# Optimization experiments

Measured on AMD Instinct MI355X. Metric: run time of the kernel, lower is better.

The kernel has to match this reference:

```python
import jax, jax.numpy as jnp
import numpy as np

N_VERT = 20000


def _gather_pad(feat, adj):
    # feat: [B, N, C]; adj: [B, N, K] with 1-based indices, 0 = padding (-> zeros)
    B, N, C = feat.shape
    padded = jnp.concatenate([jnp.zeros((B, 1, C), feat.dtype), feat], axis=1)  # [B, N+1, C]
    return jax.vmap(lambda p, a: p[a])(padded, adj)  # [B, N, K, C]


def setup_inputs() -> dict:
    key = jax.random.key(0)
    ks = jax.random.split(key, 7)
    B, N, K, M, C, O = 4, N_VERT, 16, 9, 64, 64
    x = jax.random.normal(ks[0], (B, N, C), jnp.float32)
    adj = jax.random.randint(ks[1], (B, N, K), 0, N + 1, jnp.int32)  # 0 == no neighbor
    W = jax.random.normal(ks[2], (M, O, C), jnp.float32) * 0.1
    b = jax.random.normal(ks[3], (O,), jnp.float32) * 0.1
    u = jax.random.normal(ks[4], (M, C), jnp.float32) * 0.1
    v = jax.random.normal(ks[5], (M, C), jnp.float32) * 0.1
    c = jax.random.normal(ks[6], (M,), jnp.float32) * 0.1
    return {"x": x, "adj": adj, "W": W, "b": b, "u": u, "v": v, "c": c}


def reference(x, adj, W, b, u, v, c):
    # FEAST graph conv, non-invariant path.
    mask = adj != 0  # [B, N, K]
    # attention logits: u.x_i + v.x_j + c, masked (padding) neighbors -> 0 + c
    ux = jnp.einsum('bnc,mc->bnm', x, u)          # [B, N, M]
    vx = jnp.einsum('bnc,mc->bnm', x, v)          # [B, N, M]
    vxn = _gather_pad(vx, adj)                    # [B, N, K, M]
    logits = jnp.where(mask[..., None], ux[:, :, None, :] + vxn, 0.0) + c
    q = jax.nn.softmax(logits, axis=-1)           # softmax over M kernels
    # gather raw neighbor features (zero for padding), contract q over K first,
    # then apply per-kernel W (linear, so order is equivalent to original wx-gather)
    xn = _gather_pad(x, adj)                      # [B, N, K, C]
    s = jnp.einsum('bnkm,bnkc->bnmc', q, xn)      # [B, N, M, C]
    out = jnp.einsum('bnmc,moc->bno', s, W)       # [B, N, O]
    deg = jnp.sum(mask, axis=-1).astype(x.dtype)  # [B, N]
    inv_deg = jnp.where(deg > 0, 1.0 / jnp.maximum(deg, 1.0), 0.0)
    return out * inv_deg[..., None] + b
```

## Files before the change

### kernel.cpp

```cpp
#include <hip/hip_runtime.h>
#include <cstdint>
#include <cstddef>

#define BB 4
#define NN 20000
#define KK 16
#define MM 9
#define CC 64
#define OO 64
#define BN (BB*NN)
#define MC (MM*CC)
#define UVP 12
#define QNP 160
#define QTAIL 128
#define NKS (MC/32)
#define NCHUNK16 1250

typedef _Float16 f16x8 __attribute__((ext_vector_type(8)));
typedef _Float16 f16x4 __attribute__((ext_vector_type(4)));
typedef __fp16   fp16v2 __attribute__((ext_vector_type(2)));
typedef float    f32x4 __attribute__((ext_vector_type(4)));
typedef unsigned short u16;
typedef unsigned int   u32;

union Hcv { _Float16 h; u16 u; };
__device__ __forceinline__ u16 f2h(float f) { Hcv t; t.h = (_Float16)f; return t.u; }
__device__ __forceinline__ float h2f(u16 h) { Hcv t; t.u = h; return (float)t.h; }

__global__ __launch_bounds__(256) void pre_kernel(
    const float* __restrict__ x, const float* __restrict__ W,
    const float* __restrict__ u, const float* __restrict__ v,
    const float* __restrict__ c,
    float* __restrict__ uxc, float* __restrict__ vxp,
    u16* __restrict__ xh, u16* __restrict__ wfb2)
{
    const int bid = blockIdx.x;
    if (bid >= 1250) {
        int base = (bid - 1250) * 1024 + threadIdx.x * 4;
        ushort4 wv;
        u16* wp = (u16*)&wv;
        #pragma unroll
        for (int t = 0; t < 4; ++t) {
            int i = base + t;
            int j = i & 7, o = (i >> 3) & 63, l2 = (i >> 9) & 3, ks = i >> 11;
            int kf = ks * 32 + l2 * 8 + j;
            int m = kf >> 6, cc2 = kf & 63;
            wp[t] = f2h(W[m * 4096 + o * 64 + cc2]);
        }
        *(ushort4*)(wfb2 + base) = wv;
        return;
    }
    const int wave = threadIdx.x >> 6, lane = threadIdx.x & 63;
    const int lr = lane & 15, lhi = lane >> 4;
    const int t0n = bid * 64 + wave * 16;

    const float* xr = x + (size_t)(t0n + lr) * 64 + lhi * 8;
    float xf[16];
    *(float4*)(xf + 0)  = *(const float4*)(xr + 0);
    *(float4*)(xf + 4)  = *(const float4*)(xr + 4);
    *(float4*)(xf + 8)  = *(const float4*)(xr + 32);
    *(float4*)(xf + 12) = *(const float4*)(xr + 36);
    union { u16 us[8]; f16x8 v; ushort4 s4[2]; } H0, L0, H1, L1;
    #pragma unroll
    for (int i = 0; i < 8; ++i) {
        u16 h = f2h(xf[i]);      H0.us[i] = h;  L0.us[i] = f2h(xf[i] - h2f(h));
        u16 h2 = f2h(xf[8 + i]); H1.us[i] = h2; L1.us[i] = f2h(xf[8 + i] - h2f(h2));
    }
    *(ushort4*)(xh + (size_t)(t0n + lr) * 64 + lhi * 8)      = H0.s4[0];
    *(ushort4*)(xh + (size_t)(t0n + lr) * 64 + lhi * 8 + 4)  = H0.s4[1];
    *(ushort4*)(xh + (size_t)(t0n + lr) * 64 + 32 + lhi * 8)     = H1.s4[0];
    *(ushort4*)(xh + (size_t)(t0n + lr) * 64 + 32 + lhi * 8 + 4) = H1.s4[1];

    f32x4 acc0 = {0.f,0.f,0.f,0.f}, acc1 = {0.f,0.f,0.f,0.f};
    #pragma unroll
    for (int t = 0; t < 2; ++t) {
        int r = t * 16 + lr;
        const float* gp = (r < 9) ? (u + r * 64) : (v + (r - 9) * 64);
        bool nz = r < 18;
        f32x4 acc = {0.f,0.f,0.f,0.f};
        #pragma unroll
        for (int s = 0; s < 2; ++s) {
            float gf[8];
            *(float4*)(gf + 0) = nz ? *(const float4*)(gp + s * 32 + lhi * 8)
                                    : make_float4(0.f,0.f,0.f,0.f);
            *(float4*)(gf + 4) = nz ? *(const float4*)(gp + s * 32 + lhi * 8 + 4)
                                    : make_float4(0.f,0.f,0.f,0.f);
            union { u16 us[8]; f16x8 v; } GH, GL;
            #pragma unroll
            for (int i = 0; i < 8; ++i) {
                u16 h = f2h(gf[i]); GH.us[i] = h; GL.us[i] = f2h(gf[i] - h2f(h));
            }
            f16x8 as  = s ? H1.v : H0.v;
            f16x8 asl = s ? L1.v : L0.v;
            acc = __builtin_amdgcn_mfma_f32_16x16x32_f16(as,  GH.v, acc, 0, 0, 0);
            acc = __builtin_amdgcn_mfma_f32_16x16x32_f16(as,  GL.v, acc, 0, 0, 0);
            acc = __builtin_amdgcn_mfma_f32_16x16x32_f16(asl, GH.v, acc, 0, 0, 0);
        }
        if (t == 0) acc0 = acc; else acc1 = acc;
    }
    float cv = (lr < 9) ? c[lr] : 0.f;
    #pragma unroll
    for (int reg = 0; reg < 4; ++reg) {
        int node = t0n + lhi * 4 + reg;
        if (lr < 9) uxc[(size_t)node * UVP + lr] = acc0[reg] + cv;
        else        vxp[(size_t)node * UVP + (lr - 9)] = acc0[reg];
        if (lr < 2) vxp[(size_t)node * UVP + 7 + lr] = acc1[reg];
    }
}

__global__ __launch_bounds__(256, 6) void fused_kernel(
    const u16* __restrict__ xh, const int* __restrict__ adj,
    const float* __restrict__ uxc, const float* __restrict__ vxp,
    const u16* __restrict__ wfb2, const float* __restrict__ bias,
    float* __restrict__ out)
{
    __shared__ __align__(16) u16 qlds[16 * QNP + QTAIL];
    __shared__ __align__(16) u16 slds[72 * 16 * 8];
    const int bid = blockIdx.x;
    const int grp = bid & 7;
    const int b = grp >> 1;
    const int chunk = (bid >> 3) * 2 + (grp & 1);
    const int tid = threadIdx.x, wave = tid >> 6, lane = tid & 63;
    const int lr = lane & 15, lhi = lane >> 4;
    const int node0 = b * NN + chunk * 16;
    const int rowbase = b * NN;
    const u16* xhb = xh + ((size_t)rowbase << 6);

    int jj = adj[(size_t)node0 * KK + tid];

    f16x8 aLo[4], aHi[4];
    #pragma unroll
    for (int g2 = 0; g2 < 4; ++g2) {
        int e = __builtin_amdgcn_ds_bpermute((g2 * 16 + lr) * 4, jj);
        int erow = ((e > 0) ? e : 1) - 1;
        const u16* rp = xhb + ((size_t)erow << 6) + lhi * 8;
        aLo[g2] = *(const f16x8*)(rp);
        aHi[g2] = *(const f16x8*)(rp + 32);
    }

    {
        unsigned long long bal = __ballot(jj != 0);
        int deg = __popcll((bal >> (lhi * 16)) & 0xffffull);
        float inv = (deg > 0) ? (1.0f / (float)deg) : 0.0f;
        const int node = node0 + wave * 4 + lhi;
        float q[MM];
        #pragma unroll
        for (int m = 0; m < MM; ++m) q[m] = 0.f;
        if (jj != 0) {
            const float4* ur = (const float4*)(uxc + (size_t)node * UVP);
            const float4* vr = (const float4*)(vxp + ((size_t)rowbase + (jj - 1)) * UVP);
            float4 u0 = ur[0], u1 = ur[1], u2 = ur[2];
            float4 v0 = vr[0], v1 = vr[1], v2 = vr[2];
            float l[MM] = { u0.x+v0.x, u0.y+v0.y, u0.z+v0.z, u0.w+v0.w,
                            u1.x+v1.x, u1.y+v1.y, u1.z+v1.z, u1.w+v1.w,
                            u2.x+v2.x };
            float mx = l[0];
            #pragma unroll
            for (int m = 1; m < MM; ++m) mx = fmaxf(mx, l[m]);
            float sum = 0.f;
            #pragma unroll
            for (int m = 0; m < MM; ++m) { l[m] = __expf(l[m] - mx); sum += l[m]; }
            float sc = inv / sum;
            #pragma unroll
            for (int m = 0; m < MM; ++m) q[m] = l[m] * sc;
        }
        u16* qw = qlds + (wave * 4 + lhi) * QNP + lr;
        #pragma unroll
        for (int m = 0; m < MM; ++m) qw[m * 16] = f2h(q[m]);
    }

    f16x4 qf[4];
    #pragma unroll
    for (int g2 = 0; g2 < 4; ++g2)
        qf[g2] = *(const f16x4*)(qlds + (wave * 4 + g2) * QNP + lr * 16 + lhi * 4);

    f16x8 idf[2];
    #pragma unroll
    for (int s = 0; s < 2; ++s) {
        union { u16 us[8]; f16x8 v; } t;
        #pragma unroll
        for (int j = 0; j < 8; ++j)
            t.us[j] = (lhi * 8 + j == s * 16 + lr) ? (u16)0x3C00 : (u16)0;
        idf[s] = t.v;
    }

    #pragma unroll
    for (int g2 = 0; g2 < 4; ++g2) {
        const int rnode = wave * 4 + g2;
        #pragma unroll
        for (int cc = 0; cc < 4; ++cc) {
            f32x4 xt = {0.f,0.f,0.f,0.f};
            xt = __builtin_amdgcn_mfma_f32_16x16x32_f16(
                     (cc < 2) ? aLo[g2] : aHi[g2], idf[cc & 1], xt, 0, 0, 0);
            union { fp16v2 h2[2]; f16x4 h4; } at;
            at.h2[0] = __builtin_amdgcn_cvt_pkrtz(xt[0], xt[1]);
            at.h2[1] = __builtin_amdgcn_cvt_pkrtz(xt[2], xt[3]);
            f32x4 d2 = {0.f,0.f,0.f,0.f};
            d2 = __builtin_amdgcn_mfma_f32_16x16x16f16(at.h4, qf[g2], d2, 0, 0, 0);
            if (lr < 9) {
                u32 lo = __builtin_amdgcn_perm((u32)f2h(d2[1]), (u32)f2h(d2[0]), 0x05040100u);
                u32 hi = __builtin_amdgcn_perm((u32)f2h(d2[3]), (u32)f2h(d2[2]), 0x05040100u);
                int q_ = lr * 8 + cc * 2 + (lhi >> 1);
                int idx16 = (((q_ * 16 + rnode) << 3) ^ ((lr & 7) << 3)) + (lhi & 1) * 4;
                *(uint2*)(slds + idx16) = make_uint2(lo, hi);
            }
        }
    }
    __syncthreads();

    const int o0 = wave * 16;
    float bv = bias[o0 + lr];
    f32x4 acc = {0.f,0.f,0.f,0.f};
    #pragma unroll
    for (int ks = 0; ks < NKS; ++ks) {
        int q_ = ks * 4 + lhi;
        int idx16 = ((q_ * 16 + lr) << 3) ^ (((q_ >> 3) & 7) << 3);
        f16x8 afrag = *(const f16x8*)(slds + idx16);
        f16x8 bfrag = *(const f16x8*)(wfb2 + (size_t)(((ks * 4 + lhi) * 64) + o0 + lr) * 8);
        acc = __builtin_amdgcn_mfma_f32_16x16x32_f16(afrag, bfrag, acc, 0, 0, 0);
    }
    #pragma unroll
    for (int reg = 0; reg < 4; ++reg) {
        int rr = node0 + lhi * 4 + reg;
        out[(size_t)rr * OO + o0 + lr] = acc[reg] + bv;
    }
}

extern "C" void kernel_launch(void* const* d_in, const int* in_sizes, int n_in,
                              void* d_out, int out_size, void* d_ws, size_t ws_size,
                              hipStream_t stream)
{
    const float* x   = (const float*)d_in[0];
    const int*   adj = (const int*)  d_in[1];
    const float* W   = (const float*)d_in[2];
    const float* b   = (const float*)d_in[3];
    const float* u   = (const float*)d_in[4];
    const float* v   = (const float*)d_in[5];
    const float* c   = (const float*)d_in[6];
    float* out = (float*)d_out;

    float* uxc = (float*)d_ws;
    float* vxp = uxc + (size_t)BN * UVP;
    u16*   xh  = (u16*)(vxp + (size_t)BN * UVP);
    u16*   wfb2= xh + (size_t)BN * CC;

    pre_kernel<<<1286, 256, 0, stream>>>(x, W, u, v, c, uxc, vxp, xh, wfb2);
    fused_kernel<<<5000, 256, 0, stream>>>(xh, adj, uxc, vxp, wfb2, b, out);
}
```

Measured before the change: 131.8 us.

## Fuse attention logits into main kernel and process 32 nodes per block

Moves the u·x and v·x projections out of the pre-kernel and computes the attention logits inside the fused kernel with MFMA on the already gathered fp16 neighbor rows. This removes the uxc/vxp workspace arrays and their scattered global reads. Softmax now runs across lanes with shuffles, and q is transposed through LDS with ds_read_b64_tr_b16. Each block now handles 32 nodes, so every W fragment load feeds two MFMAs and half as many blocks launch. In exchange, occupancy drops, LDS use grows, and the logits are computed in single fp16 rather than the earlier hi/lo split, which loses precision.

```diff
diff --git a/kernel.cpp b/kernel.cpp
--- a/kernel.cpp
+++ b/kernel.cpp
@@ -10,11 +10,8 @@
 #define OO 64
 #define BN (BB*NN)
 #define MC (MM*CC)
-#define UVP 12
-#define QNP 160
-#define QTAIL 128
 #define NKS (MC/32)
-#define NCHUNK16 1250
+#define NCH 625
 
 typedef _Float16 f16x8 __attribute__((ext_vector_type(8)));
 typedef _Float16 f16x4 __attribute__((ext_vector_type(4)));
@@ -25,16 +22,29 @@
 
 union Hcv { _Float16 h; u16 u; };
 __device__ __forceinline__ u16 f2h(float f) { Hcv t; t.h = (_Float16)f; return t.u; }
-__device__ __forceinline__ float h2f(u16 h) { Hcv t; t.u = h; return (float)t.h; }
 
 __global__ __launch_bounds__(256) void pre_kernel(
     const float* __restrict__ x, const float* __restrict__ W,
     const float* __restrict__ u, const float* __restrict__ v,
-    const float* __restrict__ c,
-    float* __restrict__ uxc, float* __restrict__ vxp,
-    u16* __restrict__ xh, u16* __restrict__ wfb2)
+    u16* __restrict__ xh, u16* __restrict__ wfb2, u16* __restrict__ uvfa)
 {
     const int bid = blockIdx.x;
+    if (bid == 1286) {
+        int i0 = threadIdx.x * 8;
+        u16 w8[8];
+        #pragma unroll
+        for (int tt = 0; tt < 8; ++tt) {
+            int i = i0 + tt;
+            int t = i >> 10, l = (i >> 4) & 63, s = (i >> 3) & 1, j = i & 7;
+            int m = l & 15, hh = l >> 4;
+            const float* src = t ? v : u;
+            float val = (m < 9) ? src[m * 64 + s * 32 + hh * 8 + j] : 0.f;
+            w8[tt] = f2h(val);
+        }
+        *(ushort4*)(uvfa + i0)     = *(ushort4*)(w8);
+        *(ushort4*)(uvfa + i0 + 4) = *(ushort4*)(w8 + 4);
+        return;
+    }
     if (bid >= 1250) {
         int base = (bid - 1250) * 1024 + threadIdx.x * 4;
         ushort4 wv;
@@ -53,126 +63,67 @@
     const int wave = threadIdx.x >> 6, lane = threadIdx.x & 63;
     const int lr = lane & 15, lhi = lane >> 4;
     const int t0n = bid * 64 + wave * 16;
-
     const float* xr = x + (size_t)(t0n + lr) * 64 + lhi * 8;
     float xf[16];
     *(float4*)(xf + 0)  = *(const float4*)(xr + 0);
     *(float4*)(xf + 4)  = *(const float4*)(xr + 4);
     *(float4*)(xf + 8)  = *(const float4*)(xr + 32);
     *(float4*)(xf + 12) = *(const float4*)(xr + 36);
-    union { u16 us[8]; f16x8 v; ushort4 s4[2]; } H0, L0, H1, L1;
+    union { u16 us[8]; ushort4 s4[2]; } H0, H1;
     #pragma unroll
     for (int i = 0; i < 8; ++i) {
-        u16 h = f2h(xf[i]);      H0.us[i] = h;  L0.us[i] = f2h(xf[i] - h2f(h));
-        u16 h2 = f2h(xf[8 + i]); H1.us[i] = h2; L1.us[i] = f2h(xf[8 + i] - h2f(h2));
-    }
-    *(ushort4*)(xh + (size_t)(t0n + lr) * 64 + lhi * 8)      = H0.s4[0];
-    *(ushort4*)(xh + (size_t)(t0n + lr) * 64 + lhi * 8 + 4)  = H0.s4[1];
-    *(ushort4*)(xh + (size_t)(t0n + lr) * 64 + 32 + lhi * 8)     = H1.s4[0];
-    *(ushort4*)(xh + (size_t)(t0n + lr) * 64 + 32 + lhi * 8 + 4) = H1.s4[1];
-
-    f32x4 acc0 = {0.f,0.f,0.f,0.f}, acc1 = {0.f,0.f,0.f,0.f};
-    #pragma unroll
-    for (int t = 0; t < 2; ++t) {
-        int r = t * 16 + lr;
-        const float* gp = (r < 9) ? (u + r * 64) : (v + (r - 9) * 64);
-        bool nz = r < 18;
-        f32x4 acc = {0.f,0.f,0.f,0.f};
-        #pragma unroll
-        for (int s = 0; s < 2; ++s) {
-            float gf[8];
-            *(float4*)(gf + 0) = nz ? *(const float4*)(gp + s * 32 + lhi * 8)
-                                    : make_float4(0.f,0.f,0.f,0.f);
-            *(float4*)(gf + 4) = nz ? *(const float4*)(gp + s * 32 + lhi * 8 + 4)
-                                    : make_float4(0.f,0.f,0.f,0.f);
-            union { u16 us[8]; f16x8 v; } GH, GL;
-            #pragma unroll
-            for (int i = 0; i < 8; ++i) {
-                u16 h = f2h(gf[i]); GH.us[i] = h; GL.us[i] = f2h(gf[i] - h2f(h));
-            }
-            f16x8 as  = s ? H1.v : H0.v;
-            f16x8 asl = s ? L1.v : L0.v;
-            acc = __builtin_amdgcn_mfma_f32_16x16x32_f16(as,  GH.v, acc, 0, 0, 0);
-            acc = __builtin_amdgcn_mfma_f32_16x16x32_f16(as,  GL.v, acc, 0, 0, 0);
-            acc = __builtin_amdgcn_mfma_f32_16x16x32_f16(asl, GH.v, acc, 0, 0, 0);
-        }
-        if (t == 0) acc0 = acc; else acc1 = acc;
-    }
-    float cv = (lr < 9) ? c[lr] : 0.f;
-    #pragma unroll
-    for (int reg = 0; reg < 4; ++reg) {
-        int node = t0n + lhi * 4 + reg;
-        if (lr < 9) uxc[(size_t)node * UVP + lr] = acc0[reg] + cv;
-        else        vxp[(size_t)node * UVP + (lr - 9)] = acc0[reg];
-        if (lr < 2) vxp[(size_t)node * UVP + 7 + lr] = acc1[reg];
-    }
+        H0.us[i] = f2h(xf[i]);
+        H1.us[i] = f2h(xf[8 + i]);
+    }
+    u16* xw = xh + (size_t)(t0n + lr) * 64 + lhi * 8;
+    *(ushort4*)(xw)          = H0.s4[0];
+    *(ushort4*)(xw + 4)      = H0.s4[1];
+    *(ushort4*)(xw + 32)     = H1.s4[0];
+    *(ushort4*)(xw + 32 + 4) = H1.s4[1];
 }
 
-__global__ __launch_bounds__(256, 6) void fused_kernel(
+__global__ __launch_bounds__(256, 3) void fused_kernel(
     const u16* __restrict__ xh, const int* __restrict__ adj,
-    const float* __restrict__ uxc, const float* __restrict__ vxp,
-    const u16* __restrict__ wfb2, const float* __restrict__ bias,
+    const u16* __restrict__ wfb2, const u16* __restrict__ uvfa,
+    const float* __restrict__ cvec, const float* __restrict__ bias,
     float* __restrict__ out)
 {
-    __shared__ __align__(16) u16 qlds[16 * QNP + QTAIL];
-    __shared__ __align__(16) u16 slds[72 * 16 * 8];
+    __shared__ __align__(16) u16 qlds[32 * 256];
+    __shared__ __align__(16) u16 slds[72 * 32 * 8];
     const int bid = blockIdx.x;
     const int grp = bid & 7;
     const int b = grp >> 1;
     const int chunk = (bid >> 3) * 2 + (grp & 1);
+    if (chunk >= NCH) return;
     const int tid = threadIdx.x, wave = tid >> 6, lane = tid & 63;
     const int lr = lane & 15, lhi = lane >> 4;
-    const int node0 = b * NN + chunk * 16;
-    const int rowbase = b * NN;
-    const u16* xhb = xh + ((size_t)rowbase << 6);
-
-    int jj = adj[(size_t)node0 * KK + tid];
-
-    f16x8 aLo[4], aHi[4];
-    #pragma unroll
-    for (int g2 = 0; g2 < 4; ++g2) {
-        int e = __builtin_amdgcn_ds_bpermute((g2 * 16 + lr) * 4, jj);
-        int erow = ((e > 0) ? e : 1) - 1;
-        const u16* rp = xhb + ((size_t)erow << 6) + lhi * 8;
-        aLo[g2] = *(const f16x8*)(rp);
-        aHi[g2] = *(const f16x8*)(rp + 32);
-    }
-
-    {
-        unsigned long long bal = __ballot(jj != 0);
-        int deg = __popcll((bal >> (lhi * 16)) & 0xffffull);
-        float inv = (deg > 0) ? (1.0f / (float)deg) : 0.0f;
-        const int node = node0 + wave * 4 + lhi;
-        float q[MM];
-        #pragma unroll
-        for (int m = 0; m < MM; ++m) q[m] = 0.f;
-        if (jj != 0) {
-            const float4* ur = (const float4*)(uxc + (size_t)node * UVP);
-            const float4* vr = (const float4*)(vxp + ((size_t)rowbase + (jj - 1)) * UVP);
-            float4 u0 = ur[0], u1 = ur[1], u2 = ur[2];
-            float4 v0 = vr[0], v1 = vr[1], v2 = vr[2];
-            float l[MM] = { u0.x+v0.x, u0.y+v0.y, u0.z+v0.z, u0.w+v0.w,
-                            u1.x+v1.x, u1.y+v1.y, u1.z+v1.z, u1.w+v1.w,
-                            u2.x+v2.x };
-            float mx = l[0];
-            #pragma unroll
-            for (int m = 1; m < MM; ++m) mx = fmaxf(mx, l[m]);
-            float sum = 0.f;
-            #pragma unroll
-            for (int m = 0; m < MM; ++m) { l[m] = __expf(l[m] - mx); sum += l[m]; }
-            float sc = inv / sum;
-            #pragma unroll
-            for (int m = 0; m < MM; ++m) q[m] = l[m] * sc;
-        }
-        u16* qw = qlds + (wave * 4 + lhi) * QNP + lr;
-        #pragma unroll
-        for (int m = 0; m < MM; ++m) qw[m * 16] = f2h(q[m]);
-    }
-
-    f16x4 qf[4];
-    #pragma unroll
-    for (int g2 = 0; g2 < 4; ++g2)
-        qf[g2] = *(const f16x4*)(qlds + (wave * 4 + g2) * QNP + lr * 16 + lhi * 4);
+    const int node0 = b * NN + chunk * 32;
+    const u16* xhb = xh + ((size_t)(b * NN) << 6);
+
+    int jjA[2];
+    jjA[0] = adj[(size_t)node0 * KK + tid];
+    jjA[1] = adj[(size_t)node0 * KK + 256 + tid];
+
+    f16x8 gLo[2][4], gHi[2][4];
+    #pragma unroll
+    for (int t = 0; t < 2; ++t)
+        #pragma unroll
+        for (int g2 = 0; g2 < 4; ++g2) {
+            int e = __builtin_amdgcn_ds_bpermute((g2 * 16 + lr) * 4, jjA[t]);
+            int erow = ((e > 0) ? e : 1) - 1;
+            const u16* rp = xhb + ((size_t)erow << 6) + lhi * 8;
+            gLo[t][g2] = *(const f16x8*)(rp);
+            gHi[t][g2] = *(const f16x8*)(rp + 32);
+        }
+
+    const u16* up = uvfa + lane * 16;
+    const f16x8 uAlo = *(const f16x8*)(up);
+    const f16x8 uAhi = *(const f16x8*)(up + 8);
+    const f16x8 vAlo = *(const f16x8*)(up + 1024);
+    const f16x8 vAhi = *(const f16x8*)(up + 1024 + 8);
+    float cv[4];
+    #pragma unroll
+    for (int r = 0; r < 4; ++r) { int m = lhi * 4 + r; cv[r] = (m < 9) ? cvec[m] : 0.f; }
 
     f16x8 idf[2];
     #pragma unroll
@@ -184,45 +135,97 @@
         idf[s] = t.v;
     }
 
-    #pragma unroll
-    for (int g2 = 0; g2 < 4; ++g2) {
-        const int rnode = wave * 4 + g2;
-        #pragma unroll
-        for (int cc = 0; cc < 4; ++cc) {
-            f32x4 xt = {0.f,0.f,0.f,0.f};
-            xt = __builtin_amdgcn_mfma_f32_16x16x32_f16(
-                     (cc < 2) ? aLo[g2] : aHi[g2], idf[cc & 1], xt, 0, 0, 0);
-            union { fp16v2 h2[2]; f16x4 h4; } at;
-            at.h2[0] = __builtin_amdgcn_cvt_pkrtz(xt[0], xt[1]);
-            at.h2[1] = __builtin_amdgcn_cvt_pkrtz(xt[2], xt[3]);
-            f32x4 d2 = {0.f,0.f,0.f,0.f};
-            d2 = __builtin_amdgcn_mfma_f32_16x16x16f16(at.h4, qf[g2], d2, 0, 0, 0);
-            if (lr < 9) {
-                u32 lo = __builtin_amdgcn_perm((u32)f2h(d2[1]), (u32)f2h(d2[0]), 0x05040100u);
-                u32 hi = __builtin_amdgcn_perm((u32)f2h(d2[3]), (u32)f2h(d2[2]), 0x05040100u);
-                int q_ = lr * 8 + cc * 2 + (lhi >> 1);
-                int idx16 = (((q_ * 16 + rnode) << 3) ^ ((lr & 7) << 3)) + (lhi & 1) * 4;
-                *(uint2*)(slds + idx16) = make_uint2(lo, hi);
+    const int o0 = wave * 16;
+    const float bv = bias[o0 + lr];
+    const u32 qbase = (u32)(size_t)qlds;
+
+    #pragma unroll
+    for (int t = 0; t < 2; ++t) {
+        unsigned long long bal = __ballot(jjA[t] != 0);
+        #pragma unroll
+        for (int g2 = 0; g2 < 4; ++g2) {
+            const int nd = t * 16 + wave * 4 + g2;
+            const u16* orp = xh + ((size_t)(node0 + nd) << 6) + lhi * 8;
+            f16x8 oLo = *(const f16x8*)(orp);
+            f16x8 oHi = *(const f16x8*)(orp + 32);
+            f32x4 acc = {0.f, 0.f, 0.f, 0.f};
+            acc = __builtin_amdgcn_mfma_f32_16x16x32_f16(vAlo, gLo[t][g2], acc, 0, 0, 0);
+            acc = __builtin_amdgcn_mfma_f32_16x16x32_f16(vAhi, gHi[t][g2], acc, 0, 0, 0);
+            acc = __builtin_amdgcn_mfma_f32_16x16x32_f16(uAlo, oLo, acc, 0, 0, 0);
+            acc = __builtin_amdgcn_mfma_f32_16x16x32_f16(uAhi, oHi, acc, 0, 0, 0);
+            u32 field = (u32)(bal >> (g2 * 16)) & 0xffffu;
+            int  deg  = __popc(field);
+            float inv = (deg > 0) ? __fdividef(1.0f, (float)deg) : 0.0f;
+            int kbit = (field >> lr) & 1;
+            float lm[4];
+            #pragma unroll
+            for (int r = 0; r < 4; ++r)
+                lm[r] = (lhi * 4 + r < 9) ? (acc[r] + cv[r]) : -1e30f;
+            float mx = fmaxf(fmaxf(lm[0], lm[1]), fmaxf(lm[2], lm[3]));
+            mx = fmaxf(mx, __shfl_xor(mx, 16));
+            mx = fmaxf(mx, __shfl_xor(mx, 32));
+            float p0 = __expf(lm[0] - mx), p1 = __expf(lm[1] - mx);
+            float p2 = __expf(lm[2] - mx), p3 = __expf(lm[3] - mx);
+            float S = p0 + p1 + p2 + p3;
+            S += __shfl_xor(S, 16);
+            S += __shfl_xor(S, 32);
+            float qsc = kbit ? __fdividef(inv, S) : 0.0f;
+            union { fp16v2 h2[2]; uint2 u2; } qp;
+            qp.h2[0] = __builtin_amdgcn_cvt_pkrtz(p0 * qsc, p1 * qsc);
+            qp.h2[1] = __builtin_amdgcn_cvt_pkrtz(p2 * qsc, p3 * qsc);
+            *(uint2*)(qlds + nd * 256 + lhi * 4 + (lr & 3) * 16 + (lr >> 2) * 64) = qp.u2;
+        }
+        asm volatile("s_waitcnt lgkmcnt(0)" ::: "memory");
+        f16x4 qf[4];
+        {
+            u32 qa = qbase + (u32)((t * 16 + wave * 4) * 512) + (u32)(lane * 8);
+            asm volatile("ds_read_b64_tr_b16 %0, %1 offset:0"    : "=v"(qf[0]) : "v"(qa) : "memory");
+            asm volatile("ds_read_b64_tr_b16 %0, %1 offset:512"  : "=v"(qf[1]) : "v"(qa) : "memory");
+            asm volatile("ds_read_b64_tr_b16 %0, %1 offset:1024" : "=v"(qf[2]) : "v"(qa) : "memory");
+            asm volatile("ds_read_b64_tr_b16 %0, %1 offset:1536" : "=v"(qf[3]) : "v"(qa) : "memory");
+            asm volatile("s_waitcnt lgkmcnt(0)" ::: "memory");
+            __builtin_amdgcn_sched_barrier(0);
+        }
+        #pragma unroll
+        for (int g2 = 0; g2 < 4; ++g2) {
+            const int rnode = t * 16 + wave * 4 + g2;
+            #pragma unroll
+            for (int cc = 0; cc < 4; ++cc) {
+                f32x4 xt = {0.f, 0.f, 0.f, 0.f};
+                xt = __builtin_amdgcn_mfma_f32_16x16x32_f16(
+                         (cc < 2) ? gLo[t][g2] : gHi[t][g2], idf[cc & 1], xt, 0, 0, 0);
+                union { fp16v2 h2[2]; f16x4 h4; } at;
+                at.h2[0] = __builtin_amdgcn_cvt_pkrtz(xt[0], xt[1]);
+                at.h2[1] = __builtin_amdgcn_cvt_pkrtz(xt[2], xt[3]);
+                f32x4 d2 = {0.f, 0.f, 0.f, 0.f};
+                d2 = __builtin_amdgcn_mfma_f32_16x16x16f16(at.h4, qf[g2], d2, 0, 0, 0);
+                if (lr < 9) {
+                    u32 lo = __builtin_amdgcn_perm((u32)f2h(d2[1]), (u32)f2h(d2[0]), 0x05040100u);
+                    u32 hi = __builtin_amdgcn_perm((u32)f2h(d2[3]), (u32)f2h(d2[2]), 0x05040100u);
+                    int q_ = lr * 8 + cc * 2 + (lhi >> 1);
+                    int idx = (((q_ * 32 + rnode) << 3) ^ ((lr & 7) << 3)) + (lhi & 1) * 4;
+                    *(uint2*)(slds + idx) = make_uint2(lo, hi);
+                }
             }
         }
     }
     __syncthreads();
 
-    const int o0 = wave * 16;
-    float bv = bias[o0 + lr];
-    f32x4 acc = {0.f,0.f,0.f,0.f};
+    f32x4 a0 = {0.f, 0.f, 0.f, 0.f}, a1 = {0.f, 0.f, 0.f, 0.f};
     #pragma unroll
     for (int ks = 0; ks < NKS; ++ks) {
         int q_ = ks * 4 + lhi;
-        int idx16 = ((q_ * 16 + lr) << 3) ^ (((q_ >> 3) & 7) << 3);
-        f16x8 afrag = *(const f16x8*)(slds + idx16);
-        f16x8 bfrag = *(const f16x8*)(wfb2 + (size_t)(((ks * 4 + lhi) * 64) + o0 + lr) * 8);
-        acc = __builtin_amdgcn_mfma_f32_16x16x32_f16(afrag, bfrag, acc, 0, 0, 0);
-    }
-    #pragma unroll
-    for (int reg = 0; reg < 4; ++reg) {
-        int rr = node0 + lhi * 4 + reg;
-        out[(size_t)rr * OO + o0 + lr] = acc[reg] + bv;
+        int sw = ((q_ >> 3) & 7) << 3;
+        f16x8 af0 = *(const f16x8*)(slds + ((((q_ * 32) + lr) << 3) ^ sw));
+        f16x8 af1 = *(const f16x8*)(slds + ((((q_ * 32) + 16 + lr) << 3) ^ sw));
+        f16x8 bf  = *(const f16x8*)(wfb2 + (size_t)(q_ * 64 + o0 + lr) * 8);
+        a0 = __builtin_amdgcn_mfma_f32_16x16x32_f16(af0, bf, a0, 0, 0, 0);
+        a1 = __builtin_amdgcn_mfma_f32_16x16x32_f16(af1, bf, a1, 0, 0, 0);
+    }
+    #pragma unroll
+    for (int r = 0; r < 4; ++r) {
+        out[(size_t)(node0 + lhi * 4 + r) * OO + o0 + lr]      = a0[r] + bv;
+        out[(size_t)(node0 + 16 + lhi * 4 + r) * OO + o0 + lr] = a1[r] + bv;
     }
 }
 
@@ -239,11 +242,10 @@
     const float* c   = (const float*)d_in[6];
     float* out = (float*)d_out;
 
-    float* uxc = (float*)d_ws;
-    float* vxp = uxc + (size_t)BN * UVP;
-    u16*   xh  = (u16*)(vxp + (size_t)BN * UVP);
-    u16*   wfb2= xh + (size_t)BN * CC;
-
-    pre_kernel<<<1286, 256, 0, stream>>>(x, W, u, v, c, uxc, vxp, xh, wfb2);
-    fused_kernel<<<5000, 256, 0, stream>>>(xh, adj, uxc, vxp, wfb2, b, out);
+    u16* xh   = (u16*)d_ws;
+    u16* wfb2 = xh + (size_t)BN * CC;
+    u16* uvfa = wfb2 + 36864;
+
+    pre_kernel<<<1287, 256, 0, stream>>>(x, W, u, v, xh, wfb2, uvfa);
+    fused_kernel<<<2504, 256, 0, stream>>>(xh, adj, wfb2, uvfa, c, b, out);
 }
```

Measured after the change: 134.8 us. 2.3% more time.

## Process 32 nodes per block to reuse W fragments across two node tiles

Applied to the files above, without the earlier changes.

Each fused block now handles 32 nodes instead of 16. All gathers for both 16-node halves are issued up front, and in the final GEMM each loaded W fragment feeds two MFMA accumulators. This halves how often W is read per node and amortizes block overhead. In exchange it doubles LDS and register use, lowers launch-bound occupancy from 6 to 3 blocks per CU, and launches 2504 blocks where the excess ones exit early.

```diff
diff --git a/kernel.cpp b/kernel.cpp
--- a/kernel.cpp
+++ b/kernel.cpp
@@ -14,7 +14,7 @@
 #define QNP 160
 #define QTAIL 128
 #define NKS (MC/32)
-#define NCHUNK16 1250
+#define NCH 625
 
 typedef _Float16 f16x8 __attribute__((ext_vector_type(8)));
 typedef _Float16 f16x4 __attribute__((ext_vector_type(4)));
@@ -108,71 +108,40 @@
     }
 }
 
-__global__ __launch_bounds__(256, 6) void fused_kernel(
+__global__ __launch_bounds__(256, 3) void fused_kernel(
     const u16* __restrict__ xh, const int* __restrict__ adj,
     const float* __restrict__ uxc, const float* __restrict__ vxp,
     const u16* __restrict__ wfb2, const float* __restrict__ bias,
     float* __restrict__ out)
 {
-    __shared__ __align__(16) u16 qlds[16 * QNP + QTAIL];
-    __shared__ __align__(16) u16 slds[72 * 16 * 8];
+    __shared__ __align__(16) u16 qlds[32 * QNP + QTAIL];
+    __shared__ __align__(16) u16 slds[72 * 32 * 8];
     const int bid = blockIdx.x;
     const int grp = bid & 7;
     const int b = grp >> 1;
     const int chunk = (bid >> 3) * 2 + (grp & 1);
+    if (chunk >= NCH) return;
     const int tid = threadIdx.x, wave = tid >> 6, lane = tid & 63;
     const int lr = lane & 15, lhi = lane >> 4;
-    const int node0 = b * NN + chunk * 16;
+    const int node0 = b * NN + chunk * 32;
     const int rowbase = b * NN;
     const u16* xhb = xh + ((size_t)rowbase << 6);
 
-    int jj = adj[(size_t)node0 * KK + tid];
-
-    f16x8 aLo[4], aHi[4];
-    #pragma unroll
-    for (int g2 = 0; g2 < 4; ++g2) {
-        int e = __builtin_amdgcn_ds_bpermute((g2 * 16 + lr) * 4, jj);
-        int erow = ((e > 0) ? e : 1) - 1;
-        const u16* rp = xhb + ((size_t)erow << 6) + lhi * 8;
-        aLo[g2] = *(const f16x8*)(rp);
-        aHi[g2] = *(const f16x8*)(rp + 32);
-    }
-
-    {
-        unsigned long long bal = __ballot(jj != 0);
-        int deg = __popcll((bal >> (lhi * 16)) & 0xffffull);
-        float inv = (deg > 0) ? (1.0f / (float)deg) : 0.0f;
-        const int node = node0 + wave * 4 + lhi;
-        float q[MM];
-        #pragma unroll
-        for (int m = 0; m < MM; ++m) q[m] = 0.f;
-        if (jj != 0) {
-            const float4* ur = (const float4*)(uxc + (size_t)node * UVP);
-            const float4* vr = (const float4*)(vxp + ((size_t)rowbase + (jj - 1)) * UVP);
-            float4 u0 = ur[0], u1 = ur[1], u2 = ur[2];
-            float4 v0 = vr[0], v1 = vr[1], v2 = vr[2];
-            float l[MM] = { u0.x+v0.x, u0.y+v0.y, u0.z+v0.z, u0.w+v0.w,
-                            u1.x+v1.x, u1.y+v1.y, u1.z+v1.z, u1.w+v1.w,
-                            u2.x+v2.x };
-            float mx = l[0];
-            #pragma unroll
-            for (int m = 1; m < MM; ++m) mx = fmaxf(mx, l[m]);
-            float sum = 0.f;
-            #pragma unroll
-            for (int m = 0; m < MM; ++m) { l[m] = __expf(l[m] - mx); sum += l[m]; }
-            float sc = inv / sum;
-            #pragma unroll
-            for (int m = 0; m < MM; ++m) q[m] = l[m] * sc;
-        }
-        u16* qw = qlds + (wave * 4 + lhi) * QNP + lr;
-        #pragma unroll
-        for (int m = 0; m < MM; ++m) qw[m * 16] = f2h(q[m]);
-    }
-
-    f16x4 qf[4];
-    #pragma unroll
-    for (int g2 = 0; g2 < 4; ++g2)
-        qf[g2] = *(const f16x4*)(qlds + (wave * 4 + g2) * QNP + lr * 16 + lhi * 4);
+    int jjA[2];
+    jjA[0] = adj[(size_t)node0 * KK + tid];
+    jjA[1] = adj[(size_t)node0 * KK + 256 + tid];
+
+    f16x8 gLo[2][4], gHi[2][4];
+    #pragma unroll
+    for (int t = 0; t < 2; ++t)
+        #pragma unroll
+        for (int g2 = 0; g2 < 4; ++g2) {
+            int e = __builtin_amdgcn_ds_bpermute((g2 * 16 + lr) * 4, jjA[t]);
+            int erow = ((e > 0) ? e : 1) - 1;
+            const u16* rp = xhb + ((size_t)erow << 6) + lhi * 8;
+            gLo[t][g2] = *(const f16x8*)(rp);
+            gHi[t][g2] = *(const f16x8*)(rp + 32);
+        }
 
     f16x8 idf[2];
     #pragma unroll
@@ -185,44 +154,86 @@
     }
 
     #pragma unroll
-    for (int g2 = 0; g2 < 4; ++g2) {
-        const int rnode = wave * 4 + g2;
-        #pragma unroll
-        for (int cc = 0; cc < 4; ++cc) {
-            f32x4 xt = {0.f,0.f,0.f,0.f};
-            xt = __builtin_amdgcn_mfma_f32_16x16x32_f16(
-                     (cc < 2) ? aLo[g2] : aHi[g2], idf[cc & 1], xt, 0, 0, 0);
-            union { fp16v2 h2[2]; f16x4 h4; } at;
-            at.h2[0] = __builtin_amdgcn_cvt_pkrtz(xt[0], xt[1]);
-            at.h2[1] = __builtin_amdgcn_cvt_pkrtz(xt[2], xt[3]);
-            f32x4 d2 = {0.f,0.f,0.f,0.f};
-            d2 = __builtin_amdgcn_mfma_f32_16x16x16f16(at.h4, qf[g2], d2, 0, 0, 0);
-            if (lr < 9) {
-                u32 lo = __builtin_amdgcn_perm((u32)f2h(d2[1]), (u32)f2h(d2[0]), 0x05040100u);
-                u32 hi = __builtin_amdgcn_perm((u32)f2h(d2[3]), (u32)f2h(d2[2]), 0x05040100u);
-                int q_ = lr * 8 + cc * 2 + (lhi >> 1);
-                int idx16 = (((q_ * 16 + rnode) << 3) ^ ((lr & 7) << 3)) + (lhi & 1) * 4;
-                *(uint2*)(slds + idx16) = make_uint2(lo, hi);
+    for (int t = 0; t < 2; ++t) {
+        {
+            int jj = jjA[t];
+            unsigned long long bal = __ballot(jj != 0);
+            int deg = __popcll((bal >> (lhi * 16)) & 0xffffull);
+            float inv = (deg > 0) ? (1.0f / (float)deg) : 0.0f;
+            const int node = node0 + t * 16 + wave * 4 + lhi;
+            float q[MM];
+            #pragma unroll
+            for (int m = 0; m < MM; ++m) q[m] = 0.f;
+            if (jj != 0) {
+                const float4* ur = (const float4*)(uxc + (size_t)node * UVP);
+                const float4* vr = (const float4*)(vxp + ((size_t)rowbase + (jj - 1)) * UVP);
+                float4 u0 = ur[0], u1 = ur[1], u2 = ur[2];
+                float4 v0 = vr[0], v1 = vr[1], v2 = vr[2];
+                float l[MM] = { u0.x+v0.x, u0.y+v0.y, u0.z+v0.z, u0.w+v0.w,
+                                u1.x+v1.x, u1.y+v1.y, u1.z+v1.z, u1.w+v1.w,
+                                u2.x+v2.x };
+                float mx = l[0];
+                #pragma unroll
+                for (int m = 1; m < MM; ++m) mx = fmaxf(mx, l[m]);
+                float sum = 0.f;
+                #pragma unroll
+                for (int m = 0; m < MM; ++m) { l[m] = __expf(l[m] - mx); sum += l[m]; }
+                float sc = inv / sum;
+                #pragma unroll
+                for (int m = 0; m < MM; ++m) q[m] = l[m] * sc;
             }
+            u16* qw = qlds + (t * 16 + wave * 4 + lhi) * QNP + lr;
+            #pragma unroll
+            for (int m = 0; m < MM; ++m) qw[m * 16] = f2h(q[m]);
+        }
+
+        f16x4 qf[4];
+        #pragma unroll
+        for (int g2 = 0; g2 < 4; ++g2)
+            qf[g2] = *(const f16x4*)(qlds + (t * 16 + wave * 4 + g2) * QNP + lr * 16 + lhi * 4);
+
+        #pragma unroll
+        for (int g2 = 0; g2 < 4; ++g2) {
+            const int rnode = t * 16 + wave * 4 + g2;
+            #pragma unroll
+            for (int cc = 0; cc < 4; ++cc) {
+                f32x4 xt = {0.f,0.f,0.f,0.f};
+                xt = __builtin_amdgcn_mfma_f32_16x16x32_f16(
+                         (cc < 2) ? gLo[t][g2] : gHi[t][g2], idf[cc & 1], xt, 0, 0, 0);
+                union { fp16v2 h2[2]; f16x4 h4; } at;
+                at.h2[0] = __builtin_amdgcn_cvt_pkrtz(xt[0], xt[1]);
+                at.h2[1] = __builtin_amdgcn_cvt_pkrtz(xt[2], xt[3]);
+                f32x4 d2 = {0.f,0.f,0.f,0.f};
+                d2 = __builtin_amdgcn_mfma_f32_16x16x16f16(at.h4, qf[g2], d2, 0, 0, 0);
+                if (lr < 9) {
+                    u32 lo = __builtin_amdgcn_perm((u32)f2h(d2[1]), (u32)f2h(d2[0]), 0x05040100u);
+                    u32 hi = __builtin_amdgcn_perm((u32)f2h(d2[3]), (u32)f2h(d2[2]), 0x05040100u);
+                    int q_ = lr * 8 + cc * 2 + (lhi >> 1);
+                    int idx = (((q_ * 32 + rnode) << 3) ^ ((lr & 7) << 3)) + (lhi & 1) * 4;
+                    *(uint2*)(slds + idx) = make_uint2(lo, hi);
+                }
+            }
         }
     }
     __syncthreads();
 
     const int o0 = wave * 16;
-    float bv = bias[o0 + lr];
-    f32x4 acc = {0.f,0.f,0.f,0.f};
+    const float bv = bias[o0 + lr];
+    f32x4 a0 = {0.f,0.f,0.f,0.f}, a1 = {0.f,0.f,0.f,0.f};
     #pragma unroll
     for (int ks = 0; ks < NKS; ++ks) {
         int q_ = ks * 4 + lhi;
-        int idx16 = ((q_ * 16 + lr) << 3) ^ (((q_ >> 3) & 7) << 3);
-        f16x8 afrag = *(const f16x8*)(slds + idx16);
-        f16x8 bfrag = *(const f16x8*)(wfb2 + (size_t)(((ks * 4 + lhi) * 64) + o0 + lr) * 8);
-        acc = __builtin_amdgcn_mfma_f32_16x16x32_f16(afrag, bfrag, acc, 0, 0, 0);
-    }
-    #pragma unroll
-    for (int reg = 0; reg < 4; ++reg) {
-        int rr = node0 + lhi * 4 + reg;
-        out[(size_t)rr * OO + o0 + lr] = acc[reg] + bv;
+        int sw = ((q_ >> 3) & 7) << 3;
+        f16x8 af0 = *(const f16x8*)(slds + ((((q_ * 32) + lr) << 3) ^ sw));
+        f16x8 af1 = *(const f16x8*)(slds + ((((q_ * 32) + 16 + lr) << 3) ^ sw));
+        f16x8 bf  = *(const f16x8*)(wfb2 + (size_t)(q_ * 64 + o0 + lr) * 8);
+        a0 = __builtin_amdgcn_mfma_f32_16x16x32_f16(af0, bf, a0, 0, 0, 0);
+        a1 = __builtin_amdgcn_mfma_f32_16x16x32_f16(af1, bf, a1, 0, 0, 0);
+    }
+    #pragma unroll
+    for (int r = 0; r < 4; ++r) {
+        out[(size_t)(node0 + lhi * 4 + r) * OO + o0 + lr]      = a0[r] + bv;
+        out[(size_t)(node0 + 16 + lhi * 4 + r) * OO + o0 + lr] = a1[r] + bv;
     }
 }
 
@@ -245,5 +256,5 @@
     u16*   wfb2= xh + (size_t)BN * CC;
 
     pre_kernel<<<1286, 256, 0, stream>>>(x, W, u, v, c, uxc, vxp, xh, wfb2);
-    fused_kernel<<<5000, 256, 0, stream>>>(xh, adj, uxc, vxp, wfb2, b, out);
+    fused_kernel<<<2504, 256, 0, stream>>>(xh, adj, uxc, vxp, wfb2, b, out);
 }
```

After: 135.0 us. +2.4%, slower.
